# Kernel optimization log

Hardware: AMD Instinct MI355X
Metric: run time of the kernel (lower is better)

The kernel has to match this reference:

```python
import jax, jax.numpy as jnp
import numpy as np

B, H, W = 4, 64, 64
C_IN, C_OUT = 512, 19
INTER = C_IN // 4          # 128
QK = INTER // 8            # 16
BN_EPS = 1e-3              # keras BatchNormalization default epsilon


def setup_inputs() -> dict:
    key = jax.random.key(0)
    ks = jax.random.split(key, 40)
    it = iter(range(40))

    def n(shape, s=0.05):
        return jax.random.normal(ks[next(it)], shape, jnp.float32) * s

    def bnp():
        g = 1.0 + n((INTER,), 0.1)
        b = n((INTER,), 0.1)
        m = n((INTER,), 0.1)
        v = jax.random.uniform(ks[next(it)], (INTER,), jnp.float32, 0.5, 1.5)
        return g, b, m, v

    inp = {"x": jax.random.normal(ks[next(it)], (B, H, W, C_IN), jnp.float32)}
    inp["w5a"] = n((3, 3, C_IN, INTER))
    inp["bn1_g"], inp["bn1_b"], inp["bn1_m"], inp["bn1_v"] = bnp()
    inp["wq"] = n((1, 1, INTER, QK)); inp["bq"] = n((QK,))
    inp["wk"] = n((1, 1, INTER, QK)); inp["bk"] = n((QK,))
    inp["wv"] = n((1, 1, INTER, INTER)); inp["bv"] = n((INTER,))
    inp["gamma_pam"] = jnp.float32(0.7)
    inp["w5c"] = n((3, 3, C_IN, INTER))
    inp["bn2_g"], inp["bn2_b"], inp["bn2_m"], inp["bn2_v"] = bnp()
    inp["gamma_cam"] = jnp.float32(0.6)
    inp["w51"] = n((3, 3, INTER, INTER))
    inp["bn3_g"], inp["bn3_b"], inp["bn3_m"], inp["bn3_v"] = bnp()
    inp["w52"] = n((3, 3, INTER, INTER))
    inp["bn4_g"], inp["bn4_b"], inp["bn4_m"], inp["bn4_v"] = bnp()
    inp["w8"] = n((1, 1, INTER, C_OUT))
    return inp


def _conv(x, w):
    return jax.lax.conv_general_dilated(
        x, w, (1, 1), 'SAME', dimension_numbers=('NHWC', 'HWIO', 'NHWC'))


def _bn(x, g, b, m, v):
    return (x - m) * jax.lax.rsqrt(v + BN_EPS) * g + b


def _danet_fwd(x, w5a, bn1_g, bn1_b, bn1_m, bn1_v, wq, bq, wk, bk, wv, bv,
               gamma_pam, w5c, bn2_g, bn2_b, bn2_m, bn2_v, gamma_cam,
               w51, bn3_g, bn3_b, bn3_m, bn3_v, w52, bn4_g, bn4_b, bn4_m, bn4_v, w8):
    relu = jax.nn.relu
    # --- position-attention branch ---
    feat1 = relu(_bn(_conv(x, w5a), bn1_g, bn1_b, bn1_m, bn1_v))   # [B,H,W,INTER]
    b_, h_, w_, c_ = feat1.shape
    N = h_ * w_
    q = (_conv(feat1, wq) + bq).reshape(b_, N, QK)                 # [B,N,QK]
    kk = (_conv(feat1, wk) + bk).reshape(b_, N, QK)
    vv = (_conv(feat1, wv) + bv).reshape(b_, N, c_)                # [B,N,C]
    att = jax.nn.softmax(jnp.einsum('biq,bjq->bij', q, kk), axis=-1)  # [B,N,N]
    pam = gamma_pam * jnp.einsum('bij,bjc->bic', att, vv).reshape(b_, h_, w_, c_) + feat1
    sa_conv = relu(_bn(_conv(pam, w51), bn3_g, bn3_b, bn3_m, bn3_v))
    # --- channel-attention branch ---
    feat2 = relu(_bn(_conv(x, w5c), bn2_g, bn2_b, bn2_m, bn2_v))
    xc = feat2.reshape(b_, N, c_)                                  # [B,N,C]
    energy = jnp.einsum('bnc,bnd->bcd', xc, xc)                    # [B,C,C]
    energy_new = jnp.max(energy, axis=-1, keepdims=True) - energy
    attc = jax.nn.softmax(energy_new, axis=-1)                     # [B,C,C]
    outc = jnp.einsum('bcd,bnd->bnc', attc, xc)
    cam = gamma_cam * outc.reshape(b_, h_, w_, c_) + feat2
    sc_conv = relu(_bn(_conv(cam, w52), bn4_g, bn4_b, bn4_m, bn4_v))
    # --- fusion (dropout is identity at inference) ---
    return _conv(sa_conv + sc_conv, w8)                            # [B,H,W,C_OUT]


def reference(x, w5a, bn1_g, bn1_b, bn1_m, bn1_v, wq, bq, wk, bk, wv, bv,
              gamma_pam, w5c, bn2_g, bn2_b, bn2_m, bn2_v, gamma_cam,
              w51, bn3_g, bn3_b, bn3_m, bn3_v, w52, bn4_g, bn4_b, bn4_m, bn4_v, w8):
    return _danet_fwd(x, w5a, bn1_g, bn1_b, bn1_m, bn1_v, wq, bq, wk, bk, wv, bv,
                      gamma_pam, w5c, bn2_g, bn2_b, bn2_m, bn2_v, gamma_cam,
                      w51, bn3_g, bn3_b, bn3_m, bn3_v, w52, bn4_g, bn4_b, bn4_m, bn4_v, w8)
```

## Files before the change

### kernel.cpp

```cpp
#include <hip/hip_runtime.h>

typedef unsigned short u16;
typedef unsigned int   u32;
typedef _Float16 f16;
typedef f16   f16x8 __attribute__((ext_vector_type(8)));
typedef float f32x4 __attribute__((ext_vector_type(4)));
typedef u16   u16x8 __attribute__((ext_vector_type(8)));
typedef u16   u16x4 __attribute__((ext_vector_type(4)));

#define DI __device__ __forceinline__

DI u16  f2h(float f){ f16 h = (f16)f; return __builtin_bit_cast(u16, h); }
DI float h2f(u16 u){ return (float)__builtin_bit_cast(f16, u); }
DI float hlo(u32 u){ return (float)__builtin_bit_cast(f16, (u16)(u & 0xFFFFu)); }
DI float hhi(u32 u){ return (float)__builtin_bit_cast(f16, (u16)(u >> 16)); }

DI f32x4 MFMA(f16x8 a, f16x8 b, f32x4 c){
  return __builtin_amdgcn_mfma_f32_16x16x32_f16(a, b, c, 0, 0, 0);
}

DI float dot8h(uint4 a, uint4 b){
  float s;
  s  = hlo(a.x)*hlo(b.x) + hhi(a.x)*hhi(b.x);
  s += hlo(a.y)*hlo(b.y) + hhi(a.y)*hhi(b.y);
  s += hlo(a.z)*hlo(b.z) + hhi(a.z)*hhi(b.z);
  s += hlo(a.w)*hlo(b.w) + hhi(a.w)*hhi(b.w);
  return s;
}

constexpr size_t O_XB    = 0;
constexpr size_t O_F1    = O_XB    + 16777216;
constexpr size_t O_F2H   = O_F1    + 4194304;
constexpr size_t O_F2TH  = O_F2H   + 8388608;
constexpr size_t O_ENP   = O_F2TH  + 4194304;
constexpr size_t O_Q     = O_ENP   + 4194304;
constexpr size_t O_K     = O_Q     + 1048576;
constexpr size_t O_VT    = O_K     + 1048576;
constexpr size_t O_PAM   = O_VT    + 4194304;
constexpr size_t O_CAM   = O_PAM   + 4194304;
constexpr size_t O_EN    = O_CAM   + 4194304;
constexpr size_t O_ATTC  = O_EN    + 262144;
constexpr size_t O_W5AT  = O_ATTC  + 262144;
constexpr size_t O_W5CT  = O_W5AT  + 1179648;
constexpr size_t O_W51T  = O_W5CT  + 1179648;
constexpr size_t O_W52T  = O_W51T  + 294912;
constexpr size_t O_WQT   = O_W52T  + 294912;
constexpr size_t O_WKT   = O_WQT   + 4096;
constexpr size_t O_WVT   = O_WKT   + 4096;
constexpr size_t O_W8T   = O_WVT   + 32768;
constexpr size_t O_B1    = O_W8T   + 8192;
constexpr size_t O_B2    = O_B1    + 512;
constexpr size_t O_B3    = O_B2    + 512;
constexpr size_t O_B4    = O_B3    + 512;
constexpr size_t O_SA    = O_XB;
constexpr size_t O_SC    = O_XB    + 4194304;
constexpr size_t O_OP    = O_XB;
constexpr size_t O_ML    = O_F2TH;
constexpr size_t OP_SPLIT_STRIDE = 2097152;
constexpr size_t ML_SPLIT_STRIDE = 32768;

DI void prep_w3_dev(int idx, const float* __restrict__ w, const float* __restrict__ g,
                    const float* __restrict__ bb, const float* __restrict__ m,
                    const float* __restrict__ v, u16* __restrict__ wT,
                    float* __restrict__ bias, int CIN, int lg2){
  const int n = idx & 127;
  const int rest = idx >> 7;
  const int c = rest & (CIN-1);
  const int t = rest >> lg2;
  const float s = g[n] * rsqrtf(v[n] + 1e-3f);
  wT[((size_t)(t*128 + n))*CIN + c] = f2h(w[idx] * s);
  if(rest == 0) bias[n] = bb[n] - m[n]*s;
}

DI void prep_wt_dev(int idx, const float* __restrict__ w, u16* __restrict__ wt, int K, int N){
  if(idx >= K*N) return;
  const int n = idx % N, k = idx / N;
  wt[n*K + k] = f2h(w[idx]);
}

__global__ void prep_all_k(
    const float* __restrict__ x, u16* __restrict__ xh,
    const float* w5a, const float* g1, const float* b1, const float* m1, const float* v1, u16* W5AT, float* B1,
    const float* w5c, const float* g2, const float* b2, const float* m2, const float* v2, u16* W5CT, float* B2,
    const float* w51, const float* g3, const float* b3, const float* m3, const float* v3, u16* W51T, float* B3,
    const float* w52, const float* g4, const float* b4, const float* m4, const float* v4, u16* W52T, float* B4,
    const float* wq, u16* WQT, const float* wk, u16* WKT,
    const float* wv, u16* WVT, const float* w8, u16* W8T)
{
  int bx = blockIdx.x;
  const int t = threadIdx.x;
  if(bx < 8192){
    const int i = (bx*256 + t)*4;
    const float4 v = *(const float4*)(x + i);
    xh[i] = f2h(v.x); xh[i+1] = f2h(v.y); xh[i+2] = f2h(v.z); xh[i+3] = f2h(v.w);
    return;
  }
  bx -= 8192;
  if(bx < 2304){ prep_w3_dev(bx*256+t, w5a, g1,b1,m1,v1, W5AT, B1, 512, 9); return; }
  bx -= 2304;
  if(bx < 2304){ prep_w3_dev(bx*256+t, w5c, g2,b2,m2,v2, W5CT, B2, 512, 9); return; }
  bx -= 2304;
  if(bx < 576){ prep_w3_dev(bx*256+t, w51, g3,b3,m3,v3, W51T, B3, 128, 7); return; }
  bx -= 576;
  if(bx < 576){ prep_w3_dev(bx*256+t, w52, g4,b4,m4,v4, W52T, B4, 128, 7); return; }
  bx -= 576;
  if(bx < 8){ prep_wt_dev(bx*256+t, wq, WQT, 128, 16); return; }
  bx -= 8;
  if(bx < 8){ prep_wt_dev(bx*256+t, wk, WKT, 128, 16); return; }
  bx -= 8;
  if(bx < 64){ prep_wt_dev(bx*256+t, wv, WVT, 128, 128); return; }
  bx -= 64;
  prep_wt_dev(bx*256+t, w8, W8T, 128, 19);
}

template<int CIN>
__global__ __launch_bounds__(512) void conv3x3_k(
    const u16* __restrict__ ina, const u16* __restrict__ wTa,
    const float* __restrict__ ba, u16* oha, u16* otha,
    const u16* __restrict__ inb, const u16* __restrict__ wTb,
    const float* __restrict__ bb, u16* ohb, u16* othb)
{
  __shared__ __align__(16) char SMEM[73728];

  constexpr int CPS = CIN/64;
  constexpr int S   = 9*CPS;

  const int halfsel = blockIdx.x >> 7;
  const int blk = blockIdx.x & 127;
  const u16* in  = halfsel ? inb : ina;
  const u16* wT  = halfsel ? wTb : wTa;
  const float* bias = halfsel ? bb : ba;
  u16* oh  = halfsel ? ohb : oha;
  u16* oth = halfsel ? othb : otha;

  const int tid = threadIdx.x;
  const int lane = tid & 63;
  const int wid = tid >> 6;
  const int kg = wid >> 2;
  const int wq = wid & 3;
  const int wr = wq >> 1, wc = wq & 1;
  const int l15 = lane & 15;
  const int lg = lane >> 4;
  const int rowS = tid >> 2;
  const int cst  = (tid & 3) * 16;

  const int p = blk*128 + rowS;
  const int b = p >> 12;
  const int rem = p & 4095;
  const int h = rem >> 6, w = rem & 63;

  f32x4 acc[4][4];
  #pragma unroll
  for(int i=0;i<4;++i)
    #pragma unroll
    for(int j=0;j<4;++j){ f32x4 z = {0.f,0.f,0.f,0.f}; acc[i][j] = z; }

  u16x8 ra0, ra1, rb0, rb1;
  auto LOAD = [&](int ts){
    const int tap = ts / CPS;
    const int c0 = (ts - tap*CPS)*64;
    const int dy = tap/3 - 1, dx = tap - (tap/3)*3 - 1;
    const int hh = h + dy, ww = w + dx;
    const bool valid = ((unsigned)hh < 64u) && ((unsigned)ww < 64u);
    u16x8 z = {0,0,0,0,0,0,0,0};
    ra0 = z; ra1 = z;
    if(valid){
      const u16* sp = in + (size_t)((b<<12) + (hh<<6) + ww)*CIN + c0 + cst;
      ra0 = *(const u16x8*)(sp);
      ra1 = *(const u16x8*)(sp + 8);
    }
    const u16* bp = wT + (size_t)(tap*128 + rowS)*CIN + c0 + cst;
    rb0 = *(const u16x8*)(bp);
    rb1 = *(const u16x8*)(bp + 8);
  };
  auto STORE = [&](int buf){
    u16* Ad = (u16*)(SMEM + (buf ? 18432 : 0)) + rowS*72 + cst;
    u16* Bd = (u16*)(SMEM + 36864 + (buf ? 18432 : 0)) + rowS*72 + cst;
    *(u16x8*)(Ad)     = ra0;
    *(u16x8*)(Ad + 8) = ra1;
    *(u16x8*)(Bd)     = rb0;
    *(u16x8*)(Bd + 8) = rb1;
  };

  LOAD(0); STORE(0);
  LOAD(1);
  __syncthreads();

  int cur = 0;
  const int fro = kg*32 + lg*8;
  for(int ts=0; ts<S; ++ts){
    if(ts+1 < S) STORE(cur^1);
    if(ts+2 < S) LOAD(ts+2);
    const u16* Ac = (u16*)(SMEM + (cur ? 18432 : 0));
    const u16* Bc = (u16*)(SMEM + 36864 + (cur ? 18432 : 0));
    f16x8 af[4], bf[4];
    #pragma unroll
    for(int ms=0; ms<4; ++ms)
      af[ms] = *(const f16x8*)(Ac + (wr*64 + ms*16 + l15)*72 + fro);
    #pragma unroll
    for(int ns=0; ns<4; ++ns)
      bf[ns] = *(const f16x8*)(Bc + (wc*64 + ns*16 + l15)*72 + fro);
    #pragma unroll
    for(int ms=0; ms<4; ++ms)
      #pragma unroll
      for(int ns=0; ns<4; ++ns)
        acc[ms][ns] = MFMA(af[ms], bf[ns], acc[ms][ns]);
    __syncthreads();
    cur ^= 1;
  }

  float* Mg = (float*)SMEM + wq*4096;
  if(kg){
    #pragma unroll
    for(int ms=0; ms<4; ++ms)
      #pragma unroll
      for(int ns=0; ns<4; ++ns)
        #pragma unroll
        for(int r=0; r<4; ++r)
          Mg[(ms*16 + lg*4 + r)*64 + ns*16 + l15] = acc[ms][ns][r];
  }
  __syncthreads();
  if(!kg){
    const int orow0 = blk*128 + wr*64;
    #pragma unroll
    for(int ns=0; ns<4; ++ns){
      const int col = wc*64 + ns*16 + l15;
      const float bc = bias[col];
      #pragma unroll
      for(int ms=0; ms<4; ++ms){
        const int pr0 = orow0 + ms*16 + lg*4;
        float4 vv;
        vv.x = acc[ms][ns][0] + Mg[(ms*16+lg*4+0)*64 + ns*16+l15] + bc; vv.x = vv.x > 0.f ? vv.x : 0.f;
        vv.y = acc[ms][ns][1] + Mg[(ms*16+lg*4+1)*64 + ns*16+l15] + bc; vv.y = vv.y > 0.f ? vv.y : 0.f;
        vv.z = acc[ms][ns][2] + Mg[(ms*16+lg*4+2)*64 + ns*16+l15] + bc; vv.z = vv.z > 0.f ? vv.z : 0.f;
        vv.w = acc[ms][ns][3] + Mg[(ms*16+lg*4+3)*64 + ns*16+l15] + bc; vv.w = vv.w > 0.f ? vv.w : 0.f;
        const u16 h0 = f2h(vv.x), h1 = f2h(vv.y), h2 = f2h(vv.z), h3 = f2h(vv.w);
        if(oh){
          oh[(size_t)(pr0+0)*128 + col] = h0;
          oh[(size_t)(pr0+1)*128 + col] = h1;
          oh[(size_t)(pr0+2)*128 + col] = h2;
          oh[(size_t)(pr0+3)*128 + col] = h3;
        }
        if(oth){
          const int bb2 = pr0 >> 12, pp0 = pr0 & 4095;
          u16x4 hv = {h0, h1, h2, h3};
          *(u16x4*)(oth + (size_t)(bb2*128 + col)*4096 + pp0) = hv;
        }
      }
    }
  }
}

__global__ void qk_proj_k(const u16* __restrict__ feat,
                          const u16* __restrict__ wtq, const float* __restrict__ biasq,
                          const u16* __restrict__ wtk, const float* __restrict__ biask,
                          u16* __restrict__ outq, u16* __restrict__ outk){
  const int idx = blockIdx.x*256 + threadIdx.x;
  if(idx >= 16384*16) return;
  const int n = idx & 15, p = idx >> 4;
  const u16* fr = feat + (size_t)p*128;
  const u16* wrq = wtq + n*128;
  const u16* wrk = wtk + n*128;
  float accq = biasq[n], acck = biask[n];
  #pragma unroll
  for(int k=0; k<128; k+=8){
    const uint4 f = *(const uint4*)(fr+k);
    accq += dot8h(f, *(const uint4*)(wrq+k));
    acck += dot8h(f, *(const uint4*)(wrk+k));
  }
  outq[(size_t)p*32 + n] = f2h(accq);
  outq[(size_t)p*32 + 16 + n] = 0;
  outk[(size_t)p*32 + n] = f2h(acck);
  outk[(size_t)p*32 + 16 + n] = 0;
}

__global__ __launch_bounds__(256) void v_proj_mfma_k(
    const u16* __restrict__ feat, const u16* __restrict__ wt,
    const float* __restrict__ bias, u16* __restrict__ vT)
{
  __shared__ u16 Ct[128*136];
  const int b = blockIdx.x >> 5, pb = blockIdx.x & 31;
  const int p0 = pb*128;
  const int tid = threadIdx.x;
  const int lane = tid & 63;
  const int wid = tid >> 6;
  const int wr = wid >> 1, wc = wid & 1;
  const int l15 = lane & 15;
  const int lg = lane >> 4;

  f32x4 acc[4][4];
  #pragma unroll
  for(int i=0;i<4;++i)
    #pragma unroll
    for(int j=0;j<4;++j){ f32x4 z = {0.f,0.f,0.f,0.f}; acc[i][j] = z; }

  #pragma unroll
  for(int k0=0; k0<128; k0+=32){
    f16x8 af[4], bf[4];
    #pragma unroll
    for(int ms=0; ms<4; ++ms)
      af[ms] = *(const f16x8*)(wt + (size_t)(wr*64 + ms*16 + l15)*128 + k0 + lg*8);
    #pragma unroll
    for(int ns=0; ns<4; ++ns)
      bf[ns] = *(const f16x8*)(feat + (size_t)(b*4096 + p0 + wc*64 + ns*16 + l15)*128 + k0 + lg*8);
    #pragma unroll
    for(int ms=0; ms<4; ++ms)
      #pragma unroll
      for(int ns=0; ns<4; ++ns)
        acc[ms][ns] = MFMA(af[ms], bf[ns], acc[ms][ns]);
  }
  #pragma unroll
  for(int ms=0; ms<4; ++ms){
    const int n0 = wr*64 + ms*16 + lg*4;
    #pragma unroll
    for(int r=0; r<4; ++r){
      const float bc = bias[n0 + r];
      #pragma unroll
      for(int ns=0; ns<4; ++ns)
        Ct[(n0+r)*136 + wc*64 + ns*16 + l15] = f2h(acc[ms][ns][r] + bc);
    }
  }
  __syncthreads();
  const int row = tid >> 1, half = tid & 1;
  u16* dst = vT + (size_t)(b*128 + row)*4096 + p0 + half*64;
  const u16* src = Ct + row*136 + half*64;
  #pragma unroll
  for(int j=0; j<8; ++j)
    *(u16x8*)(dst + j*8) = *(const u16x8*)(src + j*8);
}

__global__ __launch_bounds__(512) void pam_part_k(
    const u16* __restrict__ q, const u16* __restrict__ km,
    const u16* __restrict__ vT,
    u16* __restrict__ OP, float* __restrict__ ML)
{
  __shared__ u16 Vl[128*136];
  __shared__ u16 Kl[128*40];
  __shared__ u16 Pl[8*16*136];

  const int tid = threadIdx.x;
  const int lane = tid & 63;
  const int w = tid >> 6;
  const int l15 = lane & 15;
  const int lg = lane >> 4;
  const int koff = lg*8;
  const int qt = blockIdx.x;
  const int b = blockIdx.y;
  const int ks = blockIdx.z;
  const int q0 = qt*128;

  u16* Plw = Pl + w*16*136;

  const int row4 = tid >> 2, seg = tid & 3;
  const u16* vsrc = vT + (size_t)(b*128 + row4)*4096 + ks*1024 + seg*32;
  const u16* ksrc = km + (size_t)(b*4096 + ks*1024 + row4)*32 + seg*8;
  u16* vdst = Vl + row4*136 + seg*32;
  u16* kdst = Kl + row4*40 + seg*8;

  const f16x8 aQ = *(const f16x8*)(q + (size_t)(b*4096 + q0 + w*16 + l15)*32 + koff);

  float m_r[4], l_r[4];
  #pragma unroll
  for(int i=0;i<4;++i){ m_r[i] = -1e30f; l_r[i] = 0.f; }

  f32x4 accO[8];
  #pragma unroll
  for(int j=0;j<8;++j){ f32x4 z = {0.f,0.f,0.f,0.f}; accO[j] = z; }

  u16x8 rv[4], rk;
  #pragma unroll
  for(int j=0;j<4;++j) rv[j] = *(const u16x8*)(vsrc + j*8);
  rk = *(const u16x8*)(ksrc);
  #pragma unroll
  for(int j=0;j<4;++j) *(u16x8*)(vdst + j*8) = rv[j];
  *(u16x8*)(kdst) = rk;
  __syncthreads();

  const int NT = 8;
  for(int t=0; t<NT; ++t){
    if(t+1 < NT){
      vsrc += 128; ksrc += 128*32;
      #pragma unroll
      for(int j=0;j<4;++j) rv[j] = *(const u16x8*)(vsrc + j*8);
      rk = *(const u16x8*)(ksrc);
    }
    f32x4 accS[8];
    #pragma unroll
    for(int ns=0; ns<8; ++ns){
      const f16x8 bK = *(const f16x8*)(Kl + (ns*16 + l15)*40 + koff);
      f32x4 z = {0.f,0.f,0.f,0.f};
      accS[ns] = MFMA(aQ, bK, z);
    }
    float al_r[4];
    #pragma unroll
    for(int ri=0; ri<4; ++ri){
      float tmax = accS[0][ri];
      #pragma unroll
      for(int ns=1; ns<8; ++ns) tmax = fmaxf(tmax, accS[ns][ri]);
      #pragma unroll
      for(int d2=1; d2<16; d2<<=1) tmax = fmaxf(tmax, __shfl_xor(tmax, d2));
      const float mn = fmaxf(m_r[ri], tmax);
      const float al = __expf(m_r[ri] - mn);
      float ps = 0.f;
      #pragma unroll
      for(int ns=0; ns<8; ++ns){
        const float pv = __expf(accS[ns][ri] - mn);
        accS[ns][ri] = pv;
        ps += pv;
      }
      #pragma unroll
      for(int d2=1; d2<16; d2<<=1) ps += __shfl_xor(ps, d2);
      l_r[ri] = l_r[ri]*al + ps;
      m_r[ri] = mn;
      al_r[ri] = al;
    }
    #pragma unroll
    for(int ri=0; ri<4; ++ri)
      #pragma unroll
      for(int ns=0; ns<8; ++ns)
        Plw[(lg*4 + ri)*136 + ns*16 + l15] = f2h(accS[ns][ri]);
    #pragma unroll
    for(int ns=0; ns<8; ++ns)
      #pragma unroll
      for(int ri=0; ri<4; ++ri)
        accO[ns][ri] *= al_r[ri];
    #pragma unroll
    for(int kk=0; kk<4; ++kk){
      const f16x8 aP = *(const f16x8*)(Plw + l15*136 + kk*32 + koff);
      #pragma unroll
      for(int ns=0; ns<8; ++ns){
        const f16x8 bV = *(const f16x8*)(Vl + (ns*16 + l15)*136 + kk*32 + koff);
        accO[ns] = MFMA(aP, bV, accO[ns]);
      }
    }
    __syncthreads();
    if(t+1 < NT){
      #pragma unroll
      for(int j=0;j<4;++j) *(u16x8*)(vdst + j*8) = rv[j];
      *(u16x8*)(kdst) = rk;
      __syncthreads();
    }
  }

  u16* op = OP + (size_t)ks*OP_SPLIT_STRIDE + (size_t)(b*32 + qt)*16384;
  #pragma unroll
  for(int ns=0; ns<8; ++ns)
    #pragma unroll
    for(int ri=0; ri<4; ++ri)
      op[(size_t)(w*16 + lg*4 + ri)*128 + ns*16 + l15] = f2h(accO[ns][ri]);
  float* ml = ML + (size_t)ks*ML_SPLIT_STRIDE + (size_t)(b*32 + qt)*256;
  if(l15 == 0){
    #pragma unroll
    for(int ri=0; ri<4; ++ri){
      ml[(w*16 + lg*4 + ri)*2]     = m_r[ri];
      ml[(w*16 + lg*4 + ri)*2 + 1] = l_r[ri];
    }
  }
}

__global__ void pam_merge_k(const u16* __restrict__ OP, const float* __restrict__ ML,
                            const u16* __restrict__ feat1, const float* __restrict__ gpam,
                            u16* __restrict__ pam)
{
  const int idx = blockIdx.x*256 + threadIdx.x;
  const int ch = idx & 127, qg = idx >> 7;
  const int b = qg >> 12, qq = qg & 4095;
  const int qt = qq >> 7, ql = qq & 127;
  const size_t off = ((size_t)(b*32 + qt)*128 + ql)*128 + ch;
  const size_t mloff = (size_t)(b*32 + qt)*256 + ql*2;
  float m[4], l[4];
  #pragma unroll
  for(int s=0; s<4; ++s){
    m[s] = ML[s*ML_SPLIT_STRIDE + mloff];
    l[s] = ML[s*ML_SPLIT_STRIDE + mloff + 1];
  }
  const float M = fmaxf(fmaxf(m[0],m[1]), fmaxf(m[2],m[3]));
  float num = 0.f, den = 0.f;
  #pragma unroll
  for(int s=0; s<4; ++s){
    const float wgt = __expf(m[s] - M);
    num += wgt * h2f(OP[s*OP_SPLIT_STRIDE + off]);
    den += wgt * l[s];
  }
  pam[idx] = f2h(gpam[0]*num/den + h2f(feat1[idx]));
}

__global__ __launch_bounds__(256) void energy_mfma_k(const u16* __restrict__ f2T,
                                                     float* __restrict__ enp){
  __shared__ u16 Xl[128*72];
  const int b = blockIdx.x >> 4, s = blockIdx.x & 15;
  const int tid = threadIdx.x;
  const int lane = tid & 63;
  const int wid = tid >> 6;
  const int wr = wid >> 1, wc = wid & 1;
  const int l15 = lane & 15;
  const int lg = lane >> 4;
  const int rowS = tid >> 1, half = tid & 1;
  const u16* src = f2T + (size_t)(b*128 + rowS)*4096 + s*256;

  f32x4 acc[4][4];
  #pragma unroll
  for(int i=0;i<4;++i)
    #pragma unroll
    for(int j=0;j<4;++j){ f32x4 z = {0.f,0.f,0.f,0.f}; acc[i][j] = z; }

  for(int it=0; it<4; ++it){
    __syncthreads();
    const u16* sp = src + it*64 + half*32;
    const u16x8 v0 = *(const u16x8*)(sp);
    const u16x8 v1 = *(const u16x8*)(sp + 8);
    const u16x8 v2 = *(const u16x8*)(sp + 16);
    const u16x8 v3 = *(const u16x8*)(sp + 24);
    u16* dl = Xl + rowS*72 + half*32;
    *(u16x8*)(dl)      = v0;
    *(u16x8*)(dl + 8)  = v1;
    *(u16x8*)(dl + 16) = v2;
    *(u16x8*)(dl + 24) = v3;
    __syncthreads();
    #pragma unroll
    for(int kk=0; kk<2; ++kk){
      f16x8 af[4], bf[4];
      #pragma unroll
      for(int ms=0; ms<4; ++ms)
        af[ms] = *(const f16x8*)(Xl + (wr*64 + ms*16 + l15)*72 + kk*32 + lg*8);
      #pragma unroll
      for(int ns=0; ns<4; ++ns)
        bf[ns] = *(const f16x8*)(Xl + (wc*64 + ns*16 + l15)*72 + kk*32 + lg*8);
      #pragma unroll
      for(int ms=0; ms<4; ++ms)
        #pragma unroll
        for(int ns=0; ns<4; ++ns)
          acc[ms][ns] = MFMA(af[ms], bf[ns], acc[ms][ns]);
    }
  }
  float* dst = enp + (size_t)(s*4 + b)*128*128;
  #pragma unroll
  for(int ms=0; ms<4; ++ms){
    const int r0 = wr*64 + ms*16 + lg*4;
    #pragma unroll
    for(int ns=0; ns<4; ++ns){
      const int col = wc*64 + ns*16 + l15;
      #pragma unroll
      for(int r=0; r<4; ++r)
        dst[(size_t)(r0 + r)*128 + col] = acc[ms][ns][r];
    }
  }
}

__global__ __launch_bounds__(256) void attc_k(const float* __restrict__ enp, u16* __restrict__ attch){
  const int row = blockIdx.x*4 + (threadIdx.x >> 6);
  const int lane = threadIdx.x & 63;
  float e0 = 0.f, e1 = 0.f;
  const int b = row >> 7, c = row & 127;
  #pragma unroll
  for(int s=0; s<16; ++s){
    const float* base = enp + (size_t)(s*4 + b)*128*128 + (size_t)c*128;
    e0 += base[lane];
    e1 += base[64 + lane];
  }
  float mn = fminf(e0, e1);
  #pragma unroll
  for(int d2=1; d2<64; d2<<=1) mn = fminf(mn, __shfl_xor(mn, d2));
  const float p0 = __expf(mn - e0), p1 = __expf(mn - e1);
  float s = p0 + p1;
  #pragma unroll
  for(int d2=1; d2<64; d2<<=1) s += __shfl_xor(s, d2);
  const float rs = 1.f / s;
  attch[(size_t)row*128 + lane]      = f2h(p0*rs);
  attch[(size_t)row*128 + 64 + lane] = f2h(p1*rs);
}

__global__ __launch_bounds__(256) void cam_mfma_k(
    const u16* __restrict__ f2, const u16* __restrict__ attch,
    const float* __restrict__ gcam, u16* __restrict__ cam)
{
  const int b = blockIdx.x >> 5, pt = blockIdx.x & 31;
  const int tid = threadIdx.x;
  const int lane = tid & 63;
  const int wid = tid >> 6;
  const int wr = wid >> 1, wc = wid & 1;
  const int l15 = lane & 15;
  const int lg = lane >> 4;

  f32x4 acc[4][4];
  #pragma unroll
  for(int i=0;i<4;++i)
    #pragma unroll
    for(int j=0;j<4;++j){ f32x4 z = {0.f,0.f,0.f,0.f}; acc[i][j] = z; }

  #pragma unroll
  for(int k0=0; k0<128; k0+=32){
    f16x8 af[4], bf[4];
    #pragma unroll
    for(int ms=0; ms<4; ++ms)
      af[ms] = *(const f16x8*)(f2 + (size_t)(b*4096 + pt*128 + wr*64 + ms*16 + l15)*128 + k0 + lg*8);
    #pragma unroll
    for(int ns=0; ns<4; ++ns)
      bf[ns] = *(const f16x8*)(attch + (size_t)(b*128 + wc*64 + ns*16 + l15)*128 + k0 + lg*8);
    #pragma unroll
    for(int ms=0; ms<4; ++ms)
      #pragma unroll
      for(int ns=0; ns<4; ++ns)
        acc[ms][ns] = MFMA(af[ms], bf[ns], acc[ms][ns]);
  }
  const float g = gcam[0];
  #pragma unroll
  for(int ms=0; ms<4; ++ms)
    #pragma unroll
    for(int ns=0; ns<4; ++ns){
      const int col = wc*64 + ns*16 + l15;
      #pragma unroll
      for(int r=0; r<4; ++r){
        const int p = pt*128 + wr*64 + ms*16 + lg*4 + r;
        const size_t off = (size_t)(b*4096 + p)*128 + col;
        cam[off] = f2h(g*acc[ms][ns][r] + h2f(f2[off]));
      }
    }
}

__global__ void final_k(const u16* __restrict__ sa, const u16* __restrict__ sc,
                        const u16* __restrict__ w8t, float* __restrict__ out){
  const int idx = blockIdx.x*256 + threadIdx.x;
  if(idx >= 16384*19) return;
  const int p = idx / 19, n = idx - p*19;
  const u16* ra = sa + (size_t)p*128;
  const u16* rb = sc + (size_t)p*128;
  const u16* wr = w8t + (size_t)n*128;
  float acc = 0.f;
  #pragma unroll
  for(int k=0; k<128; k+=8){
    const uint4 a = *(const uint4*)(ra+k);
    const uint4 b = *(const uint4*)(rb+k);
    const uint4 w = *(const uint4*)(wr+k);
    acc += (hlo(a.x)+hlo(b.x))*hlo(w.x) + (hhi(a.x)+hhi(b.x))*hhi(w.x);
    acc += (hlo(a.y)+hlo(b.y))*hlo(w.y) + (hhi(a.y)+hhi(b.y))*hhi(w.y);
    acc += (hlo(a.z)+hlo(b.z))*hlo(w.z) + (hhi(a.z)+hhi(b.z))*hhi(w.z);
    acc += (hlo(a.w)+hlo(b.w))*hlo(w.w) + (hhi(a.w)+hhi(b.w))*hhi(w.w);
  }
  out[idx] = acc;
}

extern "C" void kernel_launch(void* const* d_in, const int* in_sizes, int n_in,
                              void* d_out, int out_size, void* d_ws, size_t ws_size,
                              hipStream_t stream)
{
  const float* x    = (const float*)d_in[0];
  const float* w5a  = (const float*)d_in[1];
  const float* bn1g = (const float*)d_in[2];
  const float* bn1b = (const float*)d_in[3];
  const float* bn1m = (const float*)d_in[4];
  const float* bn1v = (const float*)d_in[5];
  const float* wq   = (const float*)d_in[6];
  const float* bq   = (const float*)d_in[7];
  const float* wk   = (const float*)d_in[8];
  const float* bk   = (const float*)d_in[9];
  const float* wv   = (const float*)d_in[10];
  const float* bv   = (const float*)d_in[11];
  const float* gpam = (const float*)d_in[12];
  const float* w5c  = (const float*)d_in[13];
  const float* bn2g = (const float*)d_in[14];
  const float* bn2b = (const float*)d_in[15];
  const float* bn2m = (const float*)d_in[16];
  const float* bn2v = (const float*)d_in[17];
  const float* gcam = (const float*)d_in[18];
  const float* w51  = (const float*)d_in[19];
  const float* bn3g = (const float*)d_in[20];
  const float* bn3b = (const float*)d_in[21];
  const float* bn3m = (const float*)d_in[22];
  const float* bn3v = (const float*)d_in[23];
  const float* w52  = (const float*)d_in[24];
  const float* bn4g = (const float*)d_in[25];
  const float* bn4b = (const float*)d_in[26];
  const float* bn4m = (const float*)d_in[27];
  const float* bn4v = (const float*)d_in[28];
  const float* w8   = (const float*)d_in[29];

  char* ws = (char*)d_ws;
  u16*   XB    = (u16*)(ws + O_XB);
  u16*   FEAT1 = (u16*)(ws + O_F1);
  u16*   F2H   = (u16*)(ws + O_F2H);
  u16*   F2TH  = (u16*)(ws + O_F2TH);
  float* ENP   = (float*)(ws + O_ENP);
  u16*   Q     = (u16*)(ws + O_Q);
  u16*   KM    = (u16*)(ws + O_K);
  u16*   VT    = (u16*)(ws + O_VT);
  u16*   PAM   = (u16*)(ws + O_PAM);
  u16*   CAM   = (u16*)(ws + O_CAM);
  u16*   ATTCH = (u16*)(ws + O_ATTC);
  u16*   OP    = (u16*)(ws + O_OP);
  float* ML    = (float*)(ws + O_ML);
  u16*   W5AT  = (u16*)(ws + O_W5AT);
  u16*   W5CT  = (u16*)(ws + O_W5CT);
  u16*   W51T  = (u16*)(ws + O_W51T);
  u16*   W52T  = (u16*)(ws + O_W52T);
  u16*   WQT   = (u16*)(ws + O_WQT);
  u16*   WKT   = (u16*)(ws + O_WKT);
  u16*   WVT   = (u16*)(ws + O_WVT);
  u16*   W8T   = (u16*)(ws + O_W8T);
  float* B1    = (float*)(ws + O_B1);
  float* B2    = (float*)(ws + O_B2);
  float* B3    = (float*)(ws + O_B3);
  float* B4    = (float*)(ws + O_B4);
  u16*   SA    = (u16*)(ws + O_SA);
  u16*   SC    = (u16*)(ws + O_SC);
  float* OUT   = (float*)d_out;

  prep_all_k<<<14042,256,0,stream>>>(x, XB,
      w5a, bn1g,bn1b,bn1m,bn1v, W5AT, B1,
      w5c, bn2g,bn2b,bn2m,bn2v, W5CT, B2,
      w51, bn3g,bn3b,bn3m,bn3v, W51T, B3,
      w52, bn4g,bn4b,bn4m,bn4v, W52T, B4,
      wq, WQT, wk, WKT, wv, WVT, w8, W8T);

  conv3x3_k<512><<<256,512,0,stream>>>(XB, W5AT, B1, FEAT1, nullptr,
                                       XB, W5CT, B2, F2H, F2TH);

  qk_proj_k<<<1024,256,0,stream>>>(FEAT1, WQT, bq, WKT, bk, Q, KM);
  v_proj_mfma_k<<<128,256,0,stream>>>(FEAT1, WVT, bv, VT);

  energy_mfma_k<<<64,256,0,stream>>>(F2TH, ENP);
  attc_k<<<128,256,0,stream>>>(ENP, ATTCH);
  cam_mfma_k<<<128,256,0,stream>>>(F2H, ATTCH, gcam, CAM);

  pam_part_k<<<dim3(32,4,4),512,0,stream>>>(Q, KM, VT, OP, ML);
  pam_merge_k<<<8192,256,0,stream>>>(OP, ML, FEAT1, gpam, PAM);

  conv3x3_k<128><<<256,512,0,stream>>>(PAM, W51T, B3, SA, nullptr,
                                       CAM, W52T, B4, SC, nullptr);

  final_k<<<1216,256,0,stream>>>(SA, SC, W8T, OUT);
}
```

Measured before the change: 227.2 us.

## Double query rows per wave in PAM flash kernel using transposed score MFMAs

Each wave now handles 32 query rows (two 16-row fragments) instead of 16, so each block covers 256 queries and the grid is halved. Every K/V tile loaded into shared memory is reused across twice as many queries. Scores are computed transposed (K as A operand), which leaves the softmax row reductions mostly in-register, needing only two cross-lane shuffles instead of four. Probabilities are packed to fp16 pairs with cvt_pkrtz into a padded u32 shared buffer. In exchange, register pressure rises, since accO doubles to 64 floats per thread, and fewer blocks are launched (256 instead of 512), which may lower occupancy.

```diff
diff --git a/kernel.cpp b/kernel.cpp
--- a/kernel.cpp
+++ b/kernel.cpp
@@ -7,6 +7,7 @@
 typedef float f32x4 __attribute__((ext_vector_type(4)));
 typedef u16   u16x8 __attribute__((ext_vector_type(8)));
 typedef u16   u16x4 __attribute__((ext_vector_type(4)));
+typedef u32   u32x4 __attribute__((ext_vector_type(4)));
 
 #define DI __device__ __forceinline__
 
@@ -17,6 +18,12 @@
 
 DI f32x4 MFMA(f16x8 a, f16x8 b, f32x4 c){
   return __builtin_amdgcn_mfma_f32_16x16x32_f16(a, b, c, 0, 0, 0);
+}
+
+DI u32 pk2(float lo, float hi){
+  typedef __fp16 hf16x2 __attribute__((ext_vector_type(2)));
+  hf16x2 r = __builtin_amdgcn_cvt_pkrtz(lo, hi);
+  return __builtin_bit_cast(u32, r);
 }
 
 DI float dot8h(uint4 a, uint4 b){
@@ -336,20 +343,20 @@
 {
   __shared__ u16 Vl[128*136];
   __shared__ u16 Kl[128*40];
-  __shared__ u16 Pl[8*16*136];
+  __shared__ u32 Pp[8*16*66];
 
   const int tid = threadIdx.x;
   const int lane = tid & 63;
-  const int w = tid >> 6;
+  const int wv = tid >> 6;
   const int l15 = lane & 15;
   const int lg = lane >> 4;
   const int koff = lg*8;
   const int qt = blockIdx.x;
   const int b = blockIdx.y;
   const int ks = blockIdx.z;
-  const int q0 = qt*128;
-
-  u16* Plw = Pl + w*16*136;
+  const int q0 = qt*256;
+
+  u32* Pw = Pp + wv*16*66;
 
   const int row4 = tid >> 2, seg = tid & 3;
   const u16* vsrc = vT + (size_t)(b*128 + row4)*4096 + ks*1024 + seg*32;
@@ -357,15 +364,19 @@
   u16* vdst = Vl + row4*136 + seg*32;
   u16* kdst = Kl + row4*40 + seg*8;
 
-  const f16x8 aQ = *(const f16x8*)(q + (size_t)(b*4096 + q0 + w*16 + l15)*32 + koff);
-
-  float m_r[4], l_r[4];
-  #pragma unroll
-  for(int i=0;i<4;++i){ m_r[i] = -1e30f; l_r[i] = 0.f; }
-
-  f32x4 accO[8];
-  #pragma unroll
-  for(int j=0;j<8;++j){ f32x4 z = {0.f,0.f,0.f,0.f}; accO[j] = z; }
+  f16x8 aQ[2];
+  #pragma unroll
+  for(int f=0; f<2; ++f)
+    aQ[f] = *(const f16x8*)(q + (size_t)(b*4096 + q0 + wv*32 + f*16 + l15)*32 + koff);
+
+  float m_r[2] = {-1e30f, -1e30f};
+  float l_r[2] = {0.f, 0.f};
+
+  f32x4 accO[8][2];
+  #pragma unroll
+  for(int i=0;i<8;++i)
+    #pragma unroll
+    for(int f=0;f<2;++f){ f32x4 z = {0.f,0.f,0.f,0.f}; accO[i][f] = z; }
 
   u16x8 rv[4], rk;
   #pragma unroll
@@ -384,53 +395,68 @@
       for(int j=0;j<4;++j) rv[j] = *(const u16x8*)(vsrc + j*8);
       rk = *(const u16x8*)(ksrc);
     }
-    f32x4 accS[8];
+    f32x4 accST[8][2];
     #pragma unroll
     for(int ns=0; ns<8; ++ns){
-      const f16x8 bK = *(const f16x8*)(Kl + (ns*16 + l15)*40 + koff);
+      const f16x8 aK = *(const f16x8*)(Kl + (ns*16 + l15)*40 + koff);
       f32x4 z = {0.f,0.f,0.f,0.f};
-      accS[ns] = MFMA(aQ, bK, z);
-    }
-    float al_r[4];
-    #pragma unroll
-    for(int ri=0; ri<4; ++ri){
-      float tmax = accS[0][ri];
-      #pragma unroll
-      for(int ns=1; ns<8; ++ns) tmax = fmaxf(tmax, accS[ns][ri]);
-      #pragma unroll
-      for(int d2=1; d2<16; d2<<=1) tmax = fmaxf(tmax, __shfl_xor(tmax, d2));
-      const float mn = fmaxf(m_r[ri], tmax);
-      const float al = __expf(m_r[ri] - mn);
+      accST[ns][0] = MFMA(aK, aQ[0], z);
+      accST[ns][1] = MFMA(aK, aQ[1], z);
+    }
+    float al_[2];
+    #pragma unroll
+    for(int f=0; f<2; ++f){
+      float tmax = accST[0][f][0];
+      #pragma unroll
+      for(int ns=0; ns<8; ++ns)
+        #pragma unroll
+        for(int ri=0; ri<4; ++ri) tmax = fmaxf(tmax, accST[ns][f][ri]);
+      tmax = fmaxf(tmax, __shfl_xor(tmax, 16));
+      tmax = fmaxf(tmax, __shfl_xor(tmax, 32));
+      const float mn = fmaxf(m_r[f], tmax);
+      const float al = __expf(m_r[f] - mn);
       float ps = 0.f;
       #pragma unroll
+      for(int ns=0; ns<8; ++ns)
+        #pragma unroll
+        for(int ri=0; ri<4; ++ri){
+          const float pv = __expf(accST[ns][f][ri] - mn);
+          accST[ns][f][ri] = pv;
+          ps += pv;
+        }
+      ps += __shfl_xor(ps, 16);
+      ps += __shfl_xor(ps, 32);
+      l_r[f] = l_r[f]*al + ps;
+      m_r[f] = mn;
+      al_[f] = al;
+    }
+    #pragma unroll
+    for(int ns2=0; ns2<8; ++ns2)
+      #pragma unroll
+      for(int f=0; f<2; ++f)
+        #pragma unroll
+        for(int ri=0; ri<4; ++ri)
+          accO[ns2][f][ri] *= al_[f];
+    #pragma unroll
+    for(int f=0; f<2; ++f){
+      #pragma unroll
       for(int ns=0; ns<8; ++ns){
-        const float pv = __expf(accS[ns][ri] - mn);
-        accS[ns][ri] = pv;
-        ps += pv;
+        uint2 pr;
+        pr.x = pk2(accST[ns][f][0], accST[ns][f][1]);
+        pr.y = pk2(accST[ns][f][2], accST[ns][f][3]);
+        *(uint2*)(Pw + l15*66 + ns*8 + lg*2) = pr;
       }
       #pragma unroll
-      for(int d2=1; d2<16; d2<<=1) ps += __shfl_xor(ps, d2);
-      l_r[ri] = l_r[ri]*al + ps;
-      m_r[ri] = mn;
-      al_r[ri] = al;
-    }
-    #pragma unroll
-    for(int ri=0; ri<4; ++ri)
-      #pragma unroll
-      for(int ns=0; ns<8; ++ns)
-        Plw[(lg*4 + ri)*136 + ns*16 + l15] = f2h(accS[ns][ri]);
-    #pragma unroll
-    for(int ns=0; ns<8; ++ns)
-      #pragma unroll
-      for(int ri=0; ri<4; ++ri)
-        accO[ns][ri] *= al_r[ri];
-    #pragma unroll
-    for(int kk=0; kk<4; ++kk){
-      const f16x8 aP = *(const f16x8*)(Plw + l15*136 + kk*32 + koff);
-      #pragma unroll
-      for(int ns=0; ns<8; ++ns){
-        const f16x8 bV = *(const f16x8*)(Vl + (ns*16 + l15)*136 + kk*32 + koff);
-        accO[ns] = MFMA(aP, bV, accO[ns]);
+      for(int kk=0; kk<4; ++kk){
+        const uint2 ra = *(const uint2*)(Pw + l15*66 + kk*16 + lg*4);
+        const uint2 rb = *(const uint2*)(Pw + l15*66 + kk*16 + lg*4 + 2);
+        u32x4 rr; rr.x = ra.x; rr.y = ra.y; rr.z = rb.x; rr.w = rb.y;
+        const f16x8 bP = __builtin_bit_cast(f16x8, rr);
+        #pragma unroll
+        for(int ns2=0; ns2<8; ++ns2){
+          const f16x8 av = *(const f16x8*)(Vl + (ns2*16 + l15)*136 + kk*32 + koff);
+          accO[ns2][f] = MFMA(av, bP, accO[ns2][f]);
+        }
       }
     }
     __syncthreads();
@@ -442,18 +468,23 @@
     }
   }
 
-  u16* op = OP + (size_t)ks*OP_SPLIT_STRIDE + (size_t)(b*32 + qt)*16384;
-  #pragma unroll
-  for(int ns=0; ns<8; ++ns)
-    #pragma unroll
-    for(int ri=0; ri<4; ++ri)
-      op[(size_t)(w*16 + lg*4 + ri)*128 + ns*16 + l15] = f2h(accO[ns][ri]);
-  float* ml = ML + (size_t)ks*ML_SPLIT_STRIDE + (size_t)(b*32 + qt)*256;
-  if(l15 == 0){
-    #pragma unroll
-    for(int ri=0; ri<4; ++ri){
-      ml[(w*16 + lg*4 + ri)*2]     = m_r[ri];
-      ml[(w*16 + lg*4 + ri)*2 + 1] = l_r[ri];
+  u32* op32 = (u32*)(OP + (size_t)ks*OP_SPLIT_STRIDE + (size_t)(b*16 + qt)*32768);
+  #pragma unroll
+  for(int f=0; f<2; ++f){
+    const int ql = wv*32 + f*16 + l15;
+    #pragma unroll
+    for(int ns2=0; ns2<8; ++ns2)
+      #pragma unroll
+      for(int h=0; h<2; ++h)
+        op32[ql*64 + ns2*8 + lg*2 + h] = pk2(accO[ns2][f][2*h], accO[ns2][f][2*h+1]);
+  }
+  float* ml = ML + (size_t)ks*ML_SPLIT_STRIDE + (size_t)(b*16 + qt)*512;
+  if(lg == 0){
+    #pragma unroll
+    for(int f=0; f<2; ++f){
+      const int ql = wv*32 + f*16 + l15;
+      ml[ql*2]     = m_r[f];
+      ml[ql*2 + 1] = l_r[f];
     }
   }
 }
@@ -465,9 +496,9 @@
   const int idx = blockIdx.x*256 + threadIdx.x;
   const int ch = idx & 127, qg = idx >> 7;
   const int b = qg >> 12, qq = qg & 4095;
-  const int qt = qq >> 7, ql = qq & 127;
-  const size_t off = ((size_t)(b*32 + qt)*128 + ql)*128 + ch;
-  const size_t mloff = (size_t)(b*32 + qt)*256 + ql*2;
+  const int qt = qq >> 8, ql = qq & 255;
+  const size_t off = ((size_t)(b*16 + qt)*256 + ql)*128 + ch;
+  const size_t mloff = (size_t)(b*16 + qt)*512 + ql*2;
   float m[4], l[4];
   #pragma unroll
   for(int s=0; s<4; ++s){
@@ -722,7 +753,7 @@
   attc_k<<<128,256,0,stream>>>(ENP, ATTCH);
   cam_mfma_k<<<128,256,0,stream>>>(F2H, ATTCH, gcam, CAM);
 
-  pam_part_k<<<dim3(32,4,4),512,0,stream>>>(Q, KM, VT, OP, ML);
+  pam_part_k<<<dim3(16,4,4),512,0,stream>>>(Q, KM, VT, OP, ML);
   pam_merge_k<<<8192,256,0,stream>>>(OP, ML, FEAT1, gpam, PAM);
 
   conv3x3_k<128><<<256,512,0,stream>>>(PAM, W51T, B3, SA, nullptr,
```

Measured after the change: 207.7 us (median of 2 runs). 8.6% less time.
